# Performance work log

Measured on AMD Instinct MI355X. Metric: run time of the kernel, lower is better.

Reference implementation:

```python
import jax, jax.numpy as jnp
import numpy as np

S, B, D, H, E, K = 1024, 4, 1024, 16, 3, 2
DFF = 4 * D
DH = D // H


def _layernorm(x, w, b, eps=1e-5):
    mu = jnp.mean(x, axis=-1, keepdims=True)
    var = jnp.var(x, axis=-1, keepdims=True)
    return (x - mu) * jax.lax.rsqrt(var + eps) * w + b


def _quick_gelu(x):
    return x * jax.nn.sigmoid(1.702 * x)


def setup_inputs() -> dict:
    key = jax.random.key(0)
    ks = jax.random.split(key, 8)
    w = lambda k, shape: jax.random.normal(k, shape, dtype=jnp.float32) * 0.02
    return {
        "x": jax.random.normal(ks[0], (S, B, D), dtype=jnp.float32),
        "ln1_w": jnp.ones((D,), jnp.float32), "ln1_b": jnp.zeros((D,), jnp.float32),
        "ln2_w": jnp.ones((D,), jnp.float32), "ln2_b": jnp.zeros((D,), jnp.float32),
        "in_proj_w": w(ks[1], (3 * D, D)), "in_proj_b": jnp.zeros((3 * D,), jnp.float32),
        "out_proj_w": w(ks[2], (D, D)), "out_proj_b": jnp.zeros((D,), jnp.float32),
        "gate_w": w(ks[3], (E, D)),
        "fc_w": w(ks[4], (E, DFF, D)), "fc_b": jnp.zeros((E, DFF), jnp.float32),
        "proj_w": w(ks[5], (E, D, DFF)), "proj_b": jnp.zeros((E, D), jnp.float32),
    }


def _forward(x, ln1_w, ln1_b, ln2_w, ln2_b, in_proj_w, in_proj_b,
             out_proj_w, out_proj_b, gate_w, fc_w, fc_b, proj_w, proj_b):
    s, b, d = x.shape
    # --- causal self-attention (torch nn.MultiheadAttention, seq-first) ---
    h = _layernorm(x, ln1_w, ln1_b)
    qkv = h @ in_proj_w.T + in_proj_b                      # [S,B,3D]
    q, k, v = jnp.split(qkv, 3, axis=-1)
    to_bhsd = lambda t: t.reshape(s, b, H, DH).transpose(1, 2, 0, 3)  # [B,H,S,Dh]
    q, k, v = to_bhsd(q) * (DH ** -0.5), to_bhsd(k), to_bhsd(v)
    mask = jnp.where(jnp.arange(s)[:, None] >= jnp.arange(s)[None, :], 0.0, -jnp.inf)
    scores = jnp.einsum("bhqd,bhkd->bhqk", q, k) + mask    # [B,H,S,S]
    attn = jax.nn.softmax(scores, axis=-1)
    o = jnp.einsum("bhqk,bhkd->bhqd", attn, v)
    o = o.transpose(2, 0, 1, 3).reshape(s, b, d)
    x = x + (o @ out_proj_w.T + out_proj_b)

    # --- MoE routing ---
    hs = _layernorm(x, ln2_w, ln2_b)
    hs_flat = hs.reshape(-1, d)                            # [T,D], T = S*B
    router_logits = hs_flat @ gate_w.T                     # [T,E]
    rw = jax.nn.softmax(router_logits.astype(jnp.float32), axis=-1)
    top_vals, top_idx = jax.lax.top_k(rw, K)               # [T,K]
    top_vals = top_vals / jnp.sum(top_vals, axis=-1, keepdims=True)

    # dense grouped expert FFN (E=3 small, compute-all + masked combine)
    h1 = _quick_gelu(jnp.einsum("td,efd->etf", hs_flat, fc_w) + fc_b[:, None, :])
    expert_out = jnp.einsum("etf,edf->etd", h1, proj_w) + proj_b[:, None, :]  # [E,T,D]
    comb = jnp.sum(jax.nn.one_hot(top_idx, E, dtype=top_vals.dtype) * top_vals[..., None], axis=1)  # [T,E]
    final_hidden_states = jnp.einsum("te,etd->td", comb, expert_out).reshape(s, b, d)
    del final_hidden_states  # NOTE: source computes this but never uses it in the output

    gate_score = jnp.max(top_vals, axis=-1).reshape(s, b, 1)
    out = x * gate_score
    return out, router_logits


def reference(x, ln1_w, ln1_b, ln2_w, ln2_b, in_proj_w, in_proj_b,
              out_proj_w, out_proj_b, gate_w, fc_w, fc_b, proj_w, proj_b):
    return _forward(x, ln1_w, ln1_b, ln2_w, ln2_b, in_proj_w, in_proj_b,
                    out_proj_w, out_proj_b, gate_w, fc_w, fc_b, proj_w, proj_b)
```

## Files before the change

kernel.cpp:

```cpp
#include <hip/hip_runtime.h>
#include <hip/hip_bf16.h>

#define S_DIM 1024
#define B_DIM 4
#define D_DIM 1024
#define H_DIM 16
#define DH    64
#define T_DIM (S_DIM * B_DIM)
#define QKV_N (3 * D_DIM)

using bf16 = __hip_bfloat16;
typedef __attribute__((ext_vector_type(4))) float fx4;
typedef __attribute__((ext_vector_type(8))) short bx8;

__device__ __forceinline__ unsigned short f2bf(float f) {
  union { float f; unsigned int u; } cv; cv.f = f;
  unsigned int u = cv.u;
  unsigned int r = (u + 0x7FFFu + ((u >> 16) & 1u)) >> 16;
  return (unsigned short)r;
}

__device__ __forceinline__ void g2l16(const void* g, void* l) {
  __builtin_amdgcn_global_load_lds(
      (const __attribute__((address_space(1))) unsigned int*)g,
      (__attribute__((address_space(3))) unsigned int*)l, 16, 0, 0);
}

__global__ __launch_bounds__(256) void cast2_f32_bf16(
    const float* __restrict__ a, bf16* __restrict__ da, int an4,
    const float* __restrict__ b, bf16* __restrict__ db, int bn4) {
  const int i = blockIdx.x * 256 + threadIdx.x;
  const float* src; bf16* dst; int j;
  if (i < an4) { src = a; dst = da; j = i; }
  else if (i < an4 + bn4) { src = b; dst = db; j = i - an4; }
  else return;
  const fx4 v = ((const fx4*)src)[j];
  ushort4 u;
  u.x = f2bf(v[0]); u.y = f2bf(v[1]); u.z = f2bf(v[2]); u.w = f2bf(v[3]);
  ((ushort4*)dst)[j] = u;
}

__global__ __launch_bounds__(256) void ln_bf16_kernel(
    const float* __restrict__ x, const float* __restrict__ w,
    const float* __restrict__ bb, bf16* __restrict__ out) {
  const int t = blockIdx.x, tid = threadIdx.x;
  const fx4 v = ((const fx4*)(x + (size_t)t * D_DIM))[tid];
  float s  = v[0] + v[1] + v[2] + v[3];
  float ss = v[0]*v[0] + v[1]*v[1] + v[2]*v[2] + v[3]*v[3];
#pragma unroll
  for (int off = 32; off >= 1; off >>= 1) {
    s  += __shfl_xor(s, off);
    ss += __shfl_xor(ss, off);
  }
  __shared__ float red[8];
  const int wid = tid >> 6, lane = tid & 63;
  if (lane == 0) { red[wid] = s; red[4 + wid] = ss; }
  __syncthreads();
  s  = red[0] + red[1] + red[2] + red[3];
  ss = red[4] + red[5] + red[6] + red[7];
  const float mu = s * (1.f / D_DIM);
  const float rstd = rsqrtf(ss * (1.f / D_DIM) - mu * mu + 1e-5f);
  const fx4 wv = ((const fx4*)w)[tid];
  const fx4 bv = ((const fx4*)bb)[tid];
  ushort4 u;
  u.x = f2bf((v[0] - mu) * rstd * wv[0] + bv[0]);
  u.y = f2bf((v[1] - mu) * rstd * wv[1] + bv[1]);
  u.z = f2bf((v[2] - mu) * rstd * wv[2] + bv[2]);
  u.w = f2bf((v[3] - mu) * rstd * wv[3] + bv[3]);
  ((ushort4*)(out + (size_t)t * D_DIM))[tid] = u;
}

template <int EPI>
__global__ __launch_bounds__(256, 2) void gemm_bt(
    const bf16* __restrict__ A, const bf16* __restrict__ B,
    const float* __restrict__ bias, const float* __restrict__ resid,
    float* __restrict__ C, ushort* __restrict__ qkvb, int N, int K) {
  __shared__ bf16 sA[128 * 32];
  __shared__ bf16 sB[128 * 32];
  const int tid  = threadIdx.x;
  const int brow = blockIdx.y * 128;
  const int bcol = blockIdx.x * 128;
  const int wid  = tid >> 6;
  const int lane = tid & 63;
  const int wr   = wid >> 1;
  const int wc   = wid & 1;
  const int fr   = lane & 15;
  const int fk   = lane >> 4;

  fx4 acc[4][4];
#pragma unroll
  for (int i = 0; i < 4; ++i)
#pragma unroll
    for (int j = 0; j < 4; ++j) acc[i][j] = 0.f;

  const int arow = tid >> 2;
  const int acol = (tid & 3) * 8;

  for (int kt = 0; kt < K; kt += 32) {
    __syncthreads();
#pragma unroll
    for (int is = 0; is < 2; ++is) {
      const int row = is * 64 + arow;
      const int off = row * 64 + acol * 2;
      g2l16(A + (size_t)(brow + row) * K + kt + acol, (char*)sA + off);
      g2l16(B + (size_t)(bcol + row) * K + kt + acol, (char*)sB + off);
    }
    __syncthreads();

    bx8 af[4], bfr[4];
#pragma unroll
    for (int mm = 0; mm < 4; ++mm)
      af[mm] = *(const bx8*)(sA + (wr * 64 + mm * 16 + fr) * 32 + fk * 8);
#pragma unroll
    for (int nn = 0; nn < 4; ++nn)
      bfr[nn] = *(const bx8*)(sB + (wc * 64 + nn * 16 + fr) * 32 + fk * 8);
#pragma unroll
    for (int mm = 0; mm < 4; ++mm)
#pragma unroll
      for (int nn = 0; nn < 4; ++nn)
        acc[mm][nn] = __builtin_amdgcn_mfma_f32_16x16x32_bf16(
            af[mm], bfr[nn], acc[mm][nn], 0, 0, 0);
  }

  const int row0 = brow + wr * 64 + fk * 4;
  const int col0 = bcol + wc * 64 + fr;
#pragma unroll
  for (int mm = 0; mm < 4; ++mm) {
#pragma unroll
    for (int nn = 0; nn < 4; ++nn) {
      const int col = col0 + nn * 16;
      const float bv = bias[col];
      if (EPI == 1) {
#pragma unroll
        for (int rr = 0; rr < 4; ++rr) {
          const int row = row0 + mm * 16 + rr;
          C[(size_t)row * N + col] = acc[mm][nn][rr] + bv + resid[(size_t)row * N + col];
        }
      } else {
        const int which = col >> 10;
        const int rem   = col & 1023;
        const int hh    = rem >> 6;
        const int dh    = rem & 63;
        const float scale = (which == 0) ? 0.125f : 1.0f;
#pragma unroll
        for (int rr = 0; rr < 4; ++rr) {
          const int row = row0 + mm * 16 + rr;
          const int ss2 = row >> 2, bb2 = row & 3;
          const float v = (acc[mm][nn][rr] + bv) * scale;
          qkvb[(size_t)which * 4194304 +
               ((size_t)(bb2 * 16 + hh)) * 65536 + (size_t)ss2 * 64 + dh] = f2bf(v);
        }
      }
    }
  }
}

__global__ __launch_bounds__(256) void transpose_v(
    const ushort* __restrict__ v, ushort* __restrict__ vt) {
  __shared__ ushort tile[64][65];
  const int g  = blockIdx.x;
  const int bh = g >> 4, st = g & 15;
  const int s0 = st * 64;
  const int tid = threadIdx.x;
  const int r  = tid >> 2;
  const int c0 = (tid & 3) * 16;
  const ushort* src = v + (size_t)bh * 65536 + (size_t)(s0 + r) * 64 + c0;
#pragma unroll
  for (int i = 0; i < 2; ++i) {
    const bx8 d = *(const bx8*)(src + i * 8);
#pragma unroll
    for (int j = 0; j < 8; ++j) tile[r][c0 + i * 8 + j] = (ushort)d[j];
  }
  __syncthreads();
  ushort* dst = vt + (size_t)bh * 65536 + (size_t)r * 1024 + s0 + c0;
  bx8 w0, w1;
#pragma unroll
  for (int j = 0; j < 8; ++j) {
    w0[j] = (short)tile[c0 + j][r];
    w1[j] = (short)tile[c0 + 8 + j][r];
  }
  *(bx8*)dst = w0;
  *(bx8*)(dst + 8) = w1;
}

__global__ __launch_bounds__(256, 4) void attn_mfma(
    const ushort* __restrict__ qb, const ushort* __restrict__ kb,
    const ushort* __restrict__ vtb, ushort* __restrict__ ob) {
  __shared__ __align__(16) char sK[2][8192];
  __shared__ __align__(16) char sVT[2][8192];
  __shared__ __align__(16) char sP[8192];
  const int tid  = threadIdx.x;
  const int wid  = tid >> 6;
  const int lane = tid & 63;
  const int g  = blockIdx.x;
  const int u  = g >> 1;
  const int pr = u & 7;
  const int qt = (g & 1) ? (15 - pr) : pr;
  const int bh = u >> 3;
  const int b  = bh >> 4, h = bh & 15;
  const int q0 = qt * 64;
  const int fr = lane & 15;
  const int fk = lane >> 4;
  const size_t bhoff = (size_t)bh * 65536;

  const int qrow = q0 + wid * 16 + fr;
  const bx8 qf0 = *(const bx8*)(qb + bhoff + (size_t)qrow * 64 + fk * 8);
  const bx8 qf1 = *(const bx8*)(qb + bhoff + (size_t)qrow * 64 + 32 + fk * 8);
  asm volatile("s_waitcnt vmcnt(0)" ::: "memory");

  fx4 o4[4];
  float m[4], l[4];
#pragma unroll
  for (int dt = 0; dt < 4; ++dt) o4[dt] = 0.f;
#pragma unroll
  for (int rr = 0; rr < 4; ++rr) { m[rr] = -INFINITY; l[rr] = 0.f; }

  char* const sPw = sP + wid * 2048;

  auto stage = [&](int buf, int kbk) {
    const int k0 = kbk * 64;
#pragma unroll
    for (int is = 0; is < 2; ++is) {
      const int L    = is * 4096 + tid * 16;
      const int row  = L >> 7;
      const int colb = (L & 127) ^ ((row & 7) << 4);
      g2l16(kb  + bhoff + (size_t)(k0 + row) * 64 + (colb >> 1), sK[buf]  + L);
      g2l16(vtb + bhoff + (size_t)row * 1024 + k0 + (colb >> 1), sVT[buf] + L);
    }
  };

  stage(0, 0);
  int cur = 0;

  for (int kbk = 0; kbk <= qt; ++kbk) {
    const int k0 = kbk * 64;
    if (kbk < qt) {
      stage(cur ^ 1, kbk + 1);
      asm volatile("s_waitcnt vmcnt(4)" ::: "memory");
    } else {
      asm volatile("s_waitcnt vmcnt(0)" ::: "memory");
    }
    __builtin_amdgcn_s_barrier();
    asm volatile("" ::: "memory");
    const char* sKc  = sK[cur];
    const char* sVTc = sVT[cur];

    fx4 s4[4];
    __builtin_amdgcn_s_setprio(1);
#pragma unroll
    for (int kt = 0; kt < 4; ++kt) {
      const int krow = kt * 16 + fr;
      const int sw   = (krow & 7) << 4;
      const bx8 b0 = *(const bx8*)(sKc + krow * 128 + ((fk * 16) ^ sw));
      const bx8 b1 = *(const bx8*)(sKc + krow * 128 + ((64 + fk * 16) ^ sw));
      fx4 z = {0.f, 0.f, 0.f, 0.f};
      z = __builtin_amdgcn_mfma_f32_16x16x32_bf16(qf0, b0, z, 0, 0, 0);
      s4[kt] = __builtin_amdgcn_mfma_f32_16x16x32_bf16(qf1, b1, z, 0, 0, 0);
    }
    __builtin_amdgcn_s_setprio(0);

    if (kbk == qt) {
#pragma unroll
      for (int kt = 0; kt < 4; ++kt) {
        const int key = k0 + kt * 16 + fr;
#pragma unroll
        for (int rr = 0; rr < 4; ++rr) {
          const int qq = q0 + wid * 16 + fk * 4 + rr;
          if (key > qq) s4[kt][rr] = -INFINITY;
        }
      }
    }

    float pm[4];
#pragma unroll
    for (int rr = 0; rr < 4; ++rr)
      pm[rr] = fmaxf(fmaxf(s4[0][rr], s4[1][rr]), fmaxf(s4[2][rr], s4[3][rr]));
#pragma unroll
    for (int off = 1; off <= 8; off <<= 1)
#pragma unroll
      for (int rr = 0; rr < 4; ++rr)
        pm[rr] = fmaxf(pm[rr], __shfl_xor(pm[rr], off));

    bool need = false;
#pragma unroll
    for (int rr = 0; rr < 4; ++rr) need = need || (pm[rr] > m[rr] + 8.f);
    if (__any(need)) {
#pragma unroll
      for (int rr = 0; rr < 4; ++rr) {
        const float mn = fmaxf(m[rr], pm[rr]);
        const float f  = __expf(m[rr] - mn);
        m[rr] = mn;
        l[rr] *= f;
#pragma unroll
        for (int dt = 0; dt < 4; ++dt) o4[dt][rr] *= f;
      }
    }

#pragma unroll
    for (int kt = 0; kt < 4; ++kt) {
#pragma unroll
      for (int rr = 0; rr < 4; ++rr) {
        const float pv = __expf(s4[kt][rr] - m[rr]);
        l[rr] += pv;
        const int qr = fk * 4 + rr;
        *(ushort*)(sPw + ((qr * 128 + (kt * 16 + fr) * 2) ^ ((qr & 7) << 4))) = f2bf(pv);
      }
    }

    __builtin_amdgcn_s_setprio(1);
#pragma unroll
    for (int c = 0; c < 2; ++c) {
      const bx8 pa = *(const bx8*)(sPw + fr * 128 + ((c * 64 + fk * 16) ^ ((fr & 7) << 4)));
#pragma unroll
      for (int dt = 0; dt < 4; ++dt) {
        const int vrow = dt * 16 + fr;
        const bx8 vf = *(const bx8*)(sVTc + vrow * 128 + ((c * 64 + fk * 16) ^ ((vrow & 7) << 4)));
        o4[dt] = __builtin_amdgcn_mfma_f32_16x16x32_bf16(pa, vf, o4[dt], 0, 0, 0);
      }
    }
    __builtin_amdgcn_s_setprio(0);

    asm volatile("" ::: "memory");
    __builtin_amdgcn_s_barrier();
    asm volatile("" ::: "memory");
    cur ^= 1;
  }

#pragma unroll
  for (int off = 1; off <= 8; off <<= 1)
#pragma unroll
    for (int rr = 0; rr < 4; ++rr) l[rr] += __shfl_xor(l[rr], off);
#pragma unroll
  for (int rr = 0; rr < 4; ++rr) l[rr] = 1.f / l[rr];

#pragma unroll
  for (int dt = 0; dt < 4; ++dt) {
#pragma unroll
    for (int rr = 0; rr < 4; ++rr) {
      const int qq = q0 + wid * 16 + fk * 4 + rr;
      ob[((size_t)qq * 4 + b) * 1024 + h * 64 + dt * 16 + fr] =
          f2bf(o4[dt][rr] * l[rr]);
    }
  }
}

__global__ __launch_bounds__(256) void final_kernel(
    const float* __restrict__ xn, const float* __restrict__ w,
    const float* __restrict__ bb, const float* __restrict__ gw,
    float* __restrict__ out, float* __restrict__ rlog) {
  const int t = blockIdx.x, tid = threadIdx.x;
  const fx4 v = ((const fx4*)(xn + (size_t)t * D_DIM))[tid];
  float s  = v[0] + v[1] + v[2] + v[3];
  float ss = v[0]*v[0] + v[1]*v[1] + v[2]*v[2] + v[3]*v[3];
#pragma unroll
  for (int off = 32; off >= 1; off >>= 1) {
    s  += __shfl_xor(s, off);
    ss += __shfl_xor(ss, off);
  }
  __shared__ float red[8];
  __shared__ float red2[12];
  const int wid = tid >> 6, lane = tid & 63;
  if (lane == 0) { red[wid] = s; red[4 + wid] = ss; }
  __syncthreads();
  s  = red[0] + red[1] + red[2] + red[3];
  ss = red[4] + red[5] + red[6] + red[7];
  const float mu = s * (1.f / D_DIM);
  const float rstd = rsqrtf(ss * (1.f / D_DIM) - mu * mu + 1e-5f);
  const fx4 wv = ((const fx4*)w)[tid];
  const fx4 bv = ((const fx4*)bb)[tid];
  fx4 hv;
#pragma unroll
  for (int cc = 0; cc < 4; ++cc) hv[cc] = (v[cc] - mu) * rstd * wv[cc] + bv[cc];

  const fx4 w0 = ((const fx4*)(gw           ))[tid];
  const fx4 w1 = ((const fx4*)(gw +     D_DIM))[tid];
  const fx4 w2 = ((const fx4*)(gw + 2 * D_DIM))[tid];
  float g0 = hv[0]*w0[0] + hv[1]*w0[1] + hv[2]*w0[2] + hv[3]*w0[3];
  float g1 = hv[0]*w1[0] + hv[1]*w1[1] + hv[2]*w1[2] + hv[3]*w1[3];
  float g2 = hv[0]*w2[0] + hv[1]*w2[1] + hv[2]*w2[2] + hv[3]*w2[3];
#pragma unroll
  for (int off = 32; off >= 1; off >>= 1) {
    g0 += __shfl_xor(g0, off);
    g1 += __shfl_xor(g1, off);
    g2 += __shfl_xor(g2, off);
  }
  if (lane == 0) { red2[wid] = g0; red2[4 + wid] = g1; red2[8 + wid] = g2; }
  __syncthreads();
  g0 = red2[0] + red2[1] + red2[2]  + red2[3];
  g1 = red2[4] + red2[5] + red2[6]  + red2[7];
  g2 = red2[8] + red2[9] + red2[10] + red2[11];

  const float lmax = fmaxf(g0, fmaxf(g1, g2));
  const float lmin = fminf(g0, fminf(g1, g2));
  const float lmid = (g0 + g1 + g2) - lmax - lmin;
  const float gate = 1.f / (1.f + __expf(lmid - lmax));

  ((fx4*)(out + (size_t)t * D_DIM))[tid] = v * gate;
  if (tid == 0) {
    rlog[(size_t)t * 3 + 0] = g0;
    rlog[(size_t)t * 3 + 1] = g1;
    rlog[(size_t)t * 3 + 2] = g2;
  }
}

extern "C" void kernel_launch(void* const* d_in, const int* in_sizes, int n_in,
                              void* d_out, int out_size, void* d_ws, size_t ws_size,
                              hipStream_t stream) {
  (void)in_sizes; (void)n_in; (void)out_size; (void)ws_size;
  const float* x    = (const float*)d_in[0];
  const float* ln1w = (const float*)d_in[1];
  const float* ln1b = (const float*)d_in[2];
  const float* ln2w = (const float*)d_in[3];
  const float* ln2b = (const float*)d_in[4];
  const float* win  = (const float*)d_in[5];
  const float* bin  = (const float*)d_in[6];
  const float* wout = (const float*)d_in[7];
  const float* bout = (const float*)d_in[8];
  const float* gw   = (const float*)d_in[9];

  char* ws = (char*)d_ws;
  bf16*   w_in_b  = (bf16*)(ws);
  bf16*   w_out_b = (bf16*)(ws + 6291456);
  bf16*   h_b     = (bf16*)(ws + 8388608);
  ushort* o_b     = (ushort*)h_b;
  ushort* qkvb    = (ushort*)(ws + 16777216);
  ushort* q_b     = qkvb;
  ushort* k_b     = qkvb + 4194304;
  ushort* v_b     = qkvb + 8388608;
  float*  xnew    = (float*)(ws + 41943040);
  ushort* vt_b    = (ushort*)(ws + 58720256);

  float* out  = (float*)d_out;
  float* rlog = out + (size_t)T_DIM * D_DIM;

  cast2_f32_bf16<<<4096, 256, 0, stream>>>(win, w_in_b, 786432,
                                           wout, w_out_b, 262144);
  ln_bf16_kernel<<<T_DIM, 256, 0, stream>>>(x, ln1w, ln1b, h_b);
  gemm_bt<2><<<dim3(QKV_N / 128, T_DIM / 128), 256, 0, stream>>>(
      h_b, w_in_b, bin, nullptr, nullptr, qkvb, QKV_N, D_DIM);
  transpose_v<<<1024, 256, 0, stream>>>(v_b, vt_b);
  attn_mfma<<<1024, 256, 0, stream>>>(q_b, k_b, vt_b, o_b);
  gemm_bt<1><<<dim3(D_DIM / 128, T_DIM / 128), 256, 0, stream>>>(
      (const bf16*)o_b, w_out_b, bout, x, xnew, nullptr, D_DIM, D_DIM);
  final_kernel<<<T_DIM, 256, 0, stream>>>(xnew, ln2w, ln2b, gw, out, rlog);
}
```

Before: 132.6 us.

## Pair causal query tiles per block and transpose QK^T for per-lane softmax

Each attention block now processes two query tiles (pr and 15-pr) in sequence, so every block does the same amount of causal work, and the grid is halved to 512 blocks. The score MFMA swaps its operands (K as A, Q as B), so each lane owns one query row. This turns the row max and sum reductions into in-lane loops plus two cross-lane shuffles, and lets P be packed and written to LDS as 8-byte stores. The cost is fewer blocks in flight, a serial pipeline restart between the two tiles, and extra shuffles to map the rescale and normalisation factors back onto the output layout.

Result: faster. 118.5 us (-10.6%).

```diff
diff --git a/kernel.cpp b/kernel.cpp
--- a/kernel.cpp
+++ b/kernel.cpp
@@ -192,33 +192,17 @@
   const int tid  = threadIdx.x;
   const int wid  = tid >> 6;
   const int lane = tid & 63;
-  const int g  = blockIdx.x;
-  const int u  = g >> 1;
-  const int pr = u & 7;
-  const int qt = (g & 1) ? (15 - pr) : pr;
-  const int bh = u >> 3;
-  const int b  = bh >> 4, h = bh & 15;
-  const int q0 = qt * 64;
-  const int fr = lane & 15;
-  const int fk = lane >> 4;
+  const int g    = blockIdx.x;
+  const int bh   = g >> 3;
+  const int pr   = g & 7;
+  const int b    = bh >> 4, h = bh & 15;
+  const int fr   = lane & 15;
+  const int fk   = lane >> 4;
   const size_t bhoff = (size_t)bh * 65536;
-
-  const int qrow = q0 + wid * 16 + fr;
-  const bx8 qf0 = *(const bx8*)(qb + bhoff + (size_t)qrow * 64 + fk * 8);
-  const bx8 qf1 = *(const bx8*)(qb + bhoff + (size_t)qrow * 64 + 32 + fk * 8);
-  asm volatile("s_waitcnt vmcnt(0)" ::: "memory");
-
-  fx4 o4[4];
-  float m[4], l[4];
-#pragma unroll
-  for (int dt = 0; dt < 4; ++dt) o4[dt] = 0.f;
-#pragma unroll
-  for (int rr = 0; rr < 4; ++rr) { m[rr] = -INFINITY; l[rr] = 0.f; }
-
   char* const sPw = sP + wid * 2048;
-
-  auto stage = [&](int buf, int kbk) {
-    const int k0 = kbk * 64;
+  const int swp = (fr & 7) << 4;
+
+  auto stage = [&](int buf, int k0) {
 #pragma unroll
     for (int is = 0; is < 2; ++is) {
       const int L    = is * 4096 + tid * 16;
@@ -229,117 +213,132 @@
     }
   };
 
-  stage(0, 0);
-  int cur = 0;
-
-  for (int kbk = 0; kbk <= qt; ++kbk) {
-    const int k0 = kbk * 64;
-    if (kbk < qt) {
-      stage(cur ^ 1, kbk + 1);
-      asm volatile("s_waitcnt vmcnt(4)" ::: "memory");
-    } else {
-      asm volatile("s_waitcnt vmcnt(0)" ::: "memory");
+#pragma unroll 1
+  for (int tile = 0; tile < 2; ++tile) {
+    const int qt  = tile ? (15 - pr) : pr;
+    const int q0w = qt * 64 + wid * 16;
+
+    const ushort* qp = qb + bhoff + (size_t)(q0w + fr) * 64;
+    const bx8 qf0 = *(const bx8*)(qp + fk * 8);
+    const bx8 qf1 = *(const bx8*)(qp + 32 + fk * 8);
+
+    fx4 o4[4];
+    float m = -3e38f, l = 0.f;
+#pragma unroll
+    for (int dt = 0; dt < 4; ++dt) o4[dt] = 0.f;
+
+    stage(0, 0);
+    asm volatile("s_waitcnt vmcnt(0)" ::: "memory");
+    int cur = 0;
+
+#pragma unroll 1
+    for (int kbk = 0; kbk <= qt; ++kbk) {
+      if (kbk < qt) {
+        stage(cur ^ 1, (kbk + 1) * 64);
+        asm volatile("s_waitcnt vmcnt(4)" ::: "memory");
+      } else {
+        asm volatile("s_waitcnt vmcnt(0)" ::: "memory");
+      }
+      __builtin_amdgcn_s_barrier();
+      asm volatile("" ::: "memory");
+      const char* sKc  = sK[cur];
+      const char* sVTc = sVT[cur];
+
+      fx4 s4[4];
+      __builtin_amdgcn_s_setprio(1);
+#pragma unroll
+      for (int kt = 0; kt < 4; ++kt) {
+        const int krow = kt * 16 + fr;
+        const int sw   = (krow & 7) << 4;
+        const bx8 kf0 = *(const bx8*)(sKc + krow * 128 + ((fk * 16) ^ sw));
+        const bx8 kf1 = *(const bx8*)(sKc + krow * 128 + ((64 + fk * 16) ^ sw));
+        fx4 z = {0.f, 0.f, 0.f, 0.f};
+        z = __builtin_amdgcn_mfma_f32_16x16x32_bf16(kf0, qf0, z, 0, 0, 0);
+        s4[kt] = __builtin_amdgcn_mfma_f32_16x16x32_bf16(kf1, qf1, z, 0, 0, 0);
+      }
+      __builtin_amdgcn_s_setprio(0);
+
+      if (kbk == qt) {
+        const int qloc = wid * 16 + fr;
+#pragma unroll
+        for (int kt = 0; kt < 4; ++kt) {
+          const int keyb = kt * 16 + fk * 4;
+#pragma unroll
+          for (int rr = 0; rr < 4; ++rr)
+            if (keyb + rr > qloc) s4[kt][rr] = -3e38f;
+        }
+      }
+
+      float pm = s4[0][0];
+#pragma unroll
+      for (int kt = 0; kt < 4; ++kt)
+#pragma unroll
+        for (int rr = 0; rr < 4; ++rr) pm = fmaxf(pm, s4[kt][rr]);
+      pm = fmaxf(pm, __shfl_xor(pm, 16));
+      pm = fmaxf(pm, __shfl_xor(pm, 32));
+
+      if (__any(pm > m + 8.f)) {
+        const float mn = fmaxf(m, pm);
+        const float f  = __expf(m - mn);
+        m = mn;
+        l *= f;
+        float fq[4];
+#pragma unroll
+        for (int rr = 0; rr < 4; ++rr) fq[rr] = __shfl(f, fk * 4 + rr);
+#pragma unroll
+        for (int dt = 0; dt < 4; ++dt)
+#pragma unroll
+          for (int rr = 0; rr < 4; ++rr) o4[dt][rr] *= fq[rr];
+      }
+
+#pragma unroll
+      for (int kt = 0; kt < 4; ++kt) {
+        const float p0 = __expf(s4[kt][0] - m);
+        const float p1 = __expf(s4[kt][1] - m);
+        const float p2 = __expf(s4[kt][2] - m);
+        const float p3 = __expf(s4[kt][3] - m);
+        l += (p0 + p1) + (p2 + p3);
+        uint2 pk;
+        pk.x = ((unsigned)f2bf(p0)) | (((unsigned)f2bf(p1)) << 16);
+        pk.y = ((unsigned)f2bf(p2)) | (((unsigned)f2bf(p3)) << 16);
+        *(uint2*)(sPw + ((fr * 128 + kt * 32 + fk * 8) ^ swp)) = pk;
+      }
+
+      __builtin_amdgcn_s_setprio(1);
+#pragma unroll
+      for (int c = 0; c < 2; ++c) {
+        const bx8 pa = *(const bx8*)(sPw + ((fr * 128 + c * 64 + fk * 16) ^ swp));
+#pragma unroll
+        for (int dt = 0; dt < 4; ++dt) {
+          const int vrow = dt * 16 + fr;
+          const bx8 vf = *(const bx8*)(sVTc + vrow * 128 +
+                                       ((c * 64 + fk * 16) ^ ((vrow & 7) << 4)));
+          o4[dt] = __builtin_amdgcn_mfma_f32_16x16x32_bf16(pa, vf, o4[dt], 0, 0, 0);
+        }
+      }
+      __builtin_amdgcn_s_setprio(0);
+
+      asm volatile("" ::: "memory");
+      __builtin_amdgcn_s_barrier();
+      asm volatile("" ::: "memory");
+      cur ^= 1;
     }
-    __builtin_amdgcn_s_barrier();
-    asm volatile("" ::: "memory");
-    const char* sKc  = sK[cur];
-    const char* sVTc = sVT[cur];
-
-    fx4 s4[4];
-    __builtin_amdgcn_s_setprio(1);
-#pragma unroll
-    for (int kt = 0; kt < 4; ++kt) {
-      const int krow = kt * 16 + fr;
-      const int sw   = (krow & 7) << 4;
-      const bx8 b0 = *(const bx8*)(sKc + krow * 128 + ((fk * 16) ^ sw));
-      const bx8 b1 = *(const bx8*)(sKc + krow * 128 + ((64 + fk * 16) ^ sw));
-      fx4 z = {0.f, 0.f, 0.f, 0.f};
-      z = __builtin_amdgcn_mfma_f32_16x16x32_bf16(qf0, b0, z, 0, 0, 0);
-      s4[kt] = __builtin_amdgcn_mfma_f32_16x16x32_bf16(qf1, b1, z, 0, 0, 0);
-    }
-    __builtin_amdgcn_s_setprio(0);
-
-    if (kbk == qt) {
-#pragma unroll
-      for (int kt = 0; kt < 4; ++kt) {
-        const int key = k0 + kt * 16 + fr;
-#pragma unroll
-        for (int rr = 0; rr < 4; ++rr) {
-          const int qq = q0 + wid * 16 + fk * 4 + rr;
-          if (key > qq) s4[kt][rr] = -INFINITY;
-        }
-      }
-    }
-
-    float pm[4];
-#pragma unroll
-    for (int rr = 0; rr < 4; ++rr)
-      pm[rr] = fmaxf(fmaxf(s4[0][rr], s4[1][rr]), fmaxf(s4[2][rr], s4[3][rr]));
-#pragma unroll
-    for (int off = 1; off <= 8; off <<= 1)
-#pragma unroll
-      for (int rr = 0; rr < 4; ++rr)
-        pm[rr] = fmaxf(pm[rr], __shfl_xor(pm[rr], off));
-
-    bool need = false;
-#pragma unroll
-    for (int rr = 0; rr < 4; ++rr) need = need || (pm[rr] > m[rr] + 8.f);
-    if (__any(need)) {
+
+    l += __shfl_xor(l, 16);
+    l += __shfl_xor(l, 32);
+    const float linv = 1.f / l;
+    float lq[4];
+#pragma unroll
+    for (int rr = 0; rr < 4; ++rr) lq[rr] = __shfl(linv, fk * 4 + rr);
+
+#pragma unroll
+    for (int dt = 0; dt < 4; ++dt) {
 #pragma unroll
       for (int rr = 0; rr < 4; ++rr) {
-        const float mn = fmaxf(m[rr], pm[rr]);
-        const float f  = __expf(m[rr] - mn);
-        m[rr] = mn;
-        l[rr] *= f;
-#pragma unroll
-        for (int dt = 0; dt < 4; ++dt) o4[dt][rr] *= f;
-      }
-    }
-
-#pragma unroll
-    for (int kt = 0; kt < 4; ++kt) {
-#pragma unroll
-      for (int rr = 0; rr < 4; ++rr) {
-        const float pv = __expf(s4[kt][rr] - m[rr]);
-        l[rr] += pv;
-        const int qr = fk * 4 + rr;
-        *(ushort*)(sPw + ((qr * 128 + (kt * 16 + fr) * 2) ^ ((qr & 7) << 4))) = f2bf(pv);
-      }
-    }
-
-    __builtin_amdgcn_s_setprio(1);
-#pragma unroll
-    for (int c = 0; c < 2; ++c) {
-      const bx8 pa = *(const bx8*)(sPw + fr * 128 + ((c * 64 + fk * 16) ^ ((fr & 7) << 4)));
-#pragma unroll
-      for (int dt = 0; dt < 4; ++dt) {
-        const int vrow = dt * 16 + fr;
-        const bx8 vf = *(const bx8*)(sVTc + vrow * 128 + ((c * 64 + fk * 16) ^ ((vrow & 7) << 4)));
-        o4[dt] = __builtin_amdgcn_mfma_f32_16x16x32_bf16(pa, vf, o4[dt], 0, 0, 0);
-      }
-    }
-    __builtin_amdgcn_s_setprio(0);
-
-    asm volatile("" ::: "memory");
-    __builtin_amdgcn_s_barrier();
-    asm volatile("" ::: "memory");
-    cur ^= 1;
-  }
-
-#pragma unroll
-  for (int off = 1; off <= 8; off <<= 1)
-#pragma unroll
-    for (int rr = 0; rr < 4; ++rr) l[rr] += __shfl_xor(l[rr], off);
-#pragma unroll
-  for (int rr = 0; rr < 4; ++rr) l[rr] = 1.f / l[rr];
-
-#pragma unroll
-  for (int dt = 0; dt < 4; ++dt) {
-#pragma unroll
-    for (int rr = 0; rr < 4; ++rr) {
-      const int qq = q0 + wid * 16 + fk * 4 + rr;
-      ob[((size_t)qq * 4 + b) * 1024 + h * 64 + dt * 16 + fr] =
-          f2bf(o4[dt][rr] * l[rr]);
+        const int qq = q0w + fk * 4 + rr;
+        ob[((size_t)qq * 4 + b) * 1024 + h * 64 + dt * 16 + fr] =
+            f2bf(o4[dt][rr] * lq[rr]);
+      }
     }
   }
 }
@@ -439,7 +438,7 @@
   gemm_bt<2><<<dim3(QKV_N / 128, T_DIM / 128), 256, 0, stream>>>(
       h_b, w_in_b, bin, nullptr, nullptr, qkvb, QKV_N, D_DIM);
   transpose_v<<<1024, 256, 0, stream>>>(v_b, vt_b);
-  attn_mfma<<<1024, 256, 0, stream>>>(q_b, k_b, vt_b, o_b);
+  attn_mfma<<<512, 256, 0, stream>>>(q_b, k_b, vt_b, o_b);
   gemm_bt<1><<<dim3(D_DIM / 128, T_DIM / 128), 256, 0, stream>>>(
       (const bf16*)o_b, w_out_b, bout, x, xnew, nullptr, D_DIM, D_DIM);
   final_kernel<<<T_DIM, 256, 0, stream>>>(xnew, ln2w, ln2b, gw, out, rlog);
```
